# Performance work log

Measured on AMD Instinct MI355X. Metric: run time of the kernel, lower is better.

Reference implementation:

```python
import jax, jax.numpy as jnp
import numpy as np

N, D_IN, D_OUT, H = 8192, 256, 128, 2
SLOPE = 0.2
EPS = 1e-5  # InstanceNorm2d default eps


def setup_inputs() -> dict:
    key = jax.random.key(0)
    ks = jax.random.split(key, 6)
    x = jax.random.normal(ks[0], (N, D_IN), dtype=jnp.float32)
    conn_mask = jnp.where(jax.random.uniform(ks[1], (N, N)) < 0.05, 0.0, -1e9).astype(jnp.float32)
    W = jax.random.normal(ks[2], (H, D_IN, D_OUT), dtype=jnp.float32) * 0.05
    a_src = jax.random.normal(ks[3], (H, D_OUT), dtype=jnp.float32) * 0.1
    a_tgt = jax.random.normal(ks[4], (H, D_OUT), dtype=jnp.float32) * 0.1
    W_res = jax.random.normal(ks[5], (D_OUT, D_IN), dtype=jnp.float32) * 0.05
    return {"x": x, "conn_mask": conn_mask, "W": W, "a_src": a_src, "a_tgt": a_tgt, "W_res": W_res}


def reference(x, conn_mask, W, a_src, a_tgt, W_res):
    # dropout is identity in eval mode
    proj = jnp.einsum('nd,hdf->hnf', x, W)                      # [H,N,F]
    s_src = jnp.einsum('hnf,hf->hn', proj, a_src)[:, :, None]   # [H,N,1]
    s_tgt = jnp.einsum('hnf,hf->hn', proj, a_tgt)[:, None, :]   # [H,1,N]
    scores = jax.nn.leaky_relu(s_src + s_tgt, negative_slope=SLOPE)  # [H,N,N]
    attn = jax.nn.softmax(conn_mask[None] + scores, axis=1)     # softmax over dim=1 as in torch code
    vals = jnp.einsum('hmn,hnf->hmf', attn, proj)               # bmm -> [H,N,F]
    vals = vals.mean(axis=0)                                    # head mean -> [N,F]
    # InstanceNorm2d(1, affine=False) over the whole [N,F] plane, biased variance
    mu = vals.mean()
    var = jnp.mean(jnp.square(vals - mu))
    vals_norm = (vals - mu) / jnp.sqrt(var + EPS)
    out = vals_norm + x @ W_res.T                               # residual projection (no bias)
    out = jax.nn.elu(out)
    return (out, conn_mask)
```

## Files before the change

### kernel.cpp

```cpp
#include <hip/hip_runtime.h>
#include <stdint.h>

#define NN   8192
#define DIN  256
#define FF   128
#define NF   (NN*FF)
#define SLOPE 0.2f
#define EPSI  1e-5f
#define LOG2E 1.4426950408889634f

typedef float vf4 __attribute__((ext_vector_type(4)));
typedef short bf16x8 __attribute__((ext_vector_type(8)));
typedef float f32x4 __attribute__((ext_vector_type(4)));

#define OFF_PROJ   0
#define OFF_RESID  (2*NF)
#define OFF_PACKED (3*NF)
#define OFF_SS     (4*NF)
#define OFF_ST     (OFF_SS + 2*NN)
#define OFF_CSUM   (OFF_ST + 2*NN)
#define OFF_STATS  (OFF_CSUM + 2*NN)
#define OFF_NTAB   (OFF_STATS + 16)
#define OFF_VALS   (OFF_NTAB + 4*NN)
#define OFF_WT     (OFF_VALS + NF)
#define OFF_PT2    (OFF_WT + DIN*FF)
#define OFF_VPART  (OFF_PT2 + NF)

__device__ __forceinline__ float lrelu(float x) { return x >= 0.f ? x : SLOPE * x; }

__device__ __forceinline__ float exp2fast(float x) { return __builtin_amdgcn_exp2f(x); }

__device__ __forceinline__ uint32_t bfpack(float a, float b) {
  uint32_t ua = __float_as_uint(a); ua += 0x7fffu + ((ua >> 16) & 1u);
  uint32_t ub = __float_as_uint(b); ub += 0x7fffu + ((ub >> 16) & 1u);
  return (ua >> 16) | (ub & 0xffff0000u);
}

__global__ __launch_bounds__(256) void k_wt(const float* __restrict__ wres, float* __restrict__ wt) {
  int i = blockIdx.x * 256 + threadIdx.x;
  int d = i >> 7, f = i & 127;
  wt[i] = wres[f * DIN + d];
}

__global__ __launch_bounds__(256) void k_gemm(const float* __restrict__ x, const float* __restrict__ Wh,
                                              const float* __restrict__ wt, float* __restrict__ proj,
                                              float* __restrict__ resid) {
  const int h = blockIdx.y;
  const float* __restrict__ Wsrc = (h < 2) ? (Wh + h * (DIN * FF)) : wt;
  float* __restrict__ outp = (h < 2) ? (proj + h * NF) : resid;
  const int row0 = blockIdx.x * 32;
  __shared__ float xs[32 * 68];
  const int tid = threadIdx.x;
  const int ft = tid & 31, rt = tid >> 5;
  const int f0 = ft * 4, r0 = rt * 4;
  float acc[4][4];
#pragma unroll
  for (int j = 0; j < 4; ++j)
#pragma unroll
    for (int k = 0; k < 4; ++k) acc[j][k] = 0.f;

  for (int kc = 0; kc < 4; ++kc) {
    const int d0 = kc * 64;
#pragma unroll
    for (int k2 = 0; k2 < 2; ++k2) {
      int i = tid * 4 + k2 * 1024;
      int r = i >> 6, dd = i & 63;
      *(float4*)&xs[r * 68 + dd] = *(const float4*)&x[(row0 + r) * DIN + d0 + dd];
    }
    __syncthreads();
#pragma unroll
    for (int g = 0; g < 16; ++g) {
      const int dd = g * 4;
      float xr[4][4];
#pragma unroll
      for (int j = 0; j < 4; ++j) {
        float4 t = *(const float4*)&xs[(r0 + j) * 68 + dd];
        xr[j][0] = t.x; xr[j][1] = t.y; xr[j][2] = t.z; xr[j][3] = t.w;
      }
#pragma unroll
      for (int i = 0; i < 4; ++i) {
        float4 w = *(const float4*)&Wsrc[(d0 + dd + i) * FF + f0];
#pragma unroll
        for (int j = 0; j < 4; ++j) {
          float xx = xr[j][i];
          acc[j][0] += xx * w.x; acc[j][1] += xx * w.y;
          acc[j][2] += xx * w.z; acc[j][3] += xx * w.w;
        }
      }
    }
    __syncthreads();
  }
#pragma unroll
  for (int j = 0; j < 4; ++j) {
    int row = row0 + r0 + j;
    *(float4*)&outp[row * FF + f0] = make_float4(acc[j][0], acc[j][1], acc[j][2], acc[j][3]);
  }
}

__global__ __launch_bounds__(256) void k_sprep(const float* __restrict__ proj, const float* __restrict__ a_src,
                                               const float* __restrict__ a_tgt, float* __restrict__ ss,
                                               float* __restrict__ st, uint32_t* __restrict__ packed) {
  int lane = threadIdx.x & 63, wid = threadIdx.x >> 6;
  int n = blockIdx.x * 4 + wid;
  float2 q0 = *(const float2*)&proj[n * FF + 2 * lane];
  float2 q1 = *(const float2*)&proj[NF + n * FF + 2 * lane];
  float2 as0 = *(const float2*)&a_src[2 * lane];
  float2 at0 = *(const float2*)&a_tgt[2 * lane];
  float2 as1 = *(const float2*)&a_src[FF + 2 * lane];
  float2 at1 = *(const float2*)&a_tgt[FF + 2 * lane];
  float v0 = q0.x * as0.x + q0.y * as0.y;
  float v1 = q0.x * at0.x + q0.y * at0.y;
  float v2 = q1.x * as1.x + q1.y * as1.y;
  float v3 = q1.x * at1.x + q1.y * at1.y;
#pragma unroll
  for (int o = 1; o < 64; o <<= 1) {
    v0 += __shfl_xor(v0, o); v1 += __shfl_xor(v1, o);
    v2 += __shfl_xor(v2, o); v3 += __shfl_xor(v3, o);
  }
  uint2 pk;
  pk.x = bfpack(q0.x, q1.x);
  pk.y = bfpack(q0.y, q1.y);
  *(uint2*)&packed[n * FF + 2 * lane] = pk;
  if (lane == 0) { ss[n] = v0; ss[NN + n] = v2; st[n] = v1; st[NN + n] = v3; }
}

__global__ __launch_bounds__(256) void k_tpose(const uint32_t* __restrict__ packed, uint32_t* __restrict__ pt2) {
  __shared__ uint32_t sb[32][129];
  const int t = threadIdx.x, c = blockIdx.x;
  const int nl = t >> 3, fb = (t & 7) * 16;
#pragma unroll
  for (int i = 0; i < 4; ++i) {
    uint4 v = *(const uint4*)&packed[(c * 32 + nl) * FF + fb + i * 4];
    sb[nl][fb + i * 4] = v.x; sb[nl][fb + i * 4 + 1] = v.y;
    sb[nl][fb + i * 4 + 2] = v.z; sb[nl][fb + i * 4 + 3] = v.w;
  }
  __syncthreads();
  const int h = t >> 7, f = t & 127;
  uint32_t wbuf[16];
#pragma unroll
  for (int p = 0; p < 16; ++p) {
    uint32_t a = sb[2 * p][f], b = sb[2 * p + 1][f];
    wbuf[p] = h ? ((a >> 16) | (b & 0xffff0000u)) : ((a & 0xffffu) | (b << 16));
  }
  uint32_t* dst = pt2 + ((c * 2 + h) * 128 + f) * 16;
#pragma unroll
  for (int i = 0; i < 4; ++i)
    *(uint4*)&dst[i * 4] = make_uint4(wbuf[i * 4], wbuf[i * 4 + 1], wbuf[i * 4 + 2], wbuf[i * 4 + 3]);
}

__global__ __launch_bounds__(256) void k_scan(const float* __restrict__ mask, float* __restrict__ maskout,
                                              const float* __restrict__ ss, const float* __restrict__ st,
                                              float* __restrict__ csum, uint32_t* __restrict__ bitmask) {
  const int tid = threadIdx.x;
  const int lane = tid & 63, wv = tid >> 6;
  const int n = blockIdx.x * 256 + tid;
  const int m0 = blockIdx.y * 128;
  const int wbase = blockIdx.x * 8 + wv * 2;
  const float st0 = st[n] * LOG2E, st1 = st[NN + n] * LOG2E;
  const float ssA = ss[m0 + lane] * LOG2E,      ssB = ss[m0 + 64 + lane] * LOG2E;
  const float ssC = ss[NN + m0 + lane] * LOG2E, ssD = ss[NN + m0 + 64 + lane] * LOG2E;
  float c0 = 0.f, c1 = 0.f;

  for (int i = 0; i < 128; i += 8) {
    float v[8];
#pragma unroll
    for (int r = 0; r < 8; ++r)
      v[r] = __builtin_nontemporal_load(&mask[(size_t)(m0 + i + r) * NN + n]);
#pragma unroll
    for (int r = 0; r < 8; ++r) {
      const int m = m0 + i + r;
      __builtin_nontemporal_store(v[r], &maskout[(size_t)m * NN + n]);
      bool e = v[r] > -0.5e9f;
      unsigned long long bm = __ballot(e);
      if (lane == 0)
        *(uint2*)&bitmask[m * 256 + wbase] = make_uint2((uint32_t)bm, (uint32_t)(bm >> 32));
      const int ri = i + r;
      float s0 = __uint_as_float(__builtin_amdgcn_readlane(
                   __float_as_uint(ri < 64 ? ssA : ssB), ri & 63));
      float s1 = __uint_as_float(__builtin_amdgcn_readlane(
                   __float_as_uint(ri < 64 ? ssC : ssD), ri & 63));
      float w0 = exp2fast(lrelu(s0 + st0));
      float w1 = exp2fast(lrelu(s1 + st1));
      c0 += e ? w0 : 0.f;
      c1 += e ? w1 : 0.f;
    }
  }
  atomicAdd(&csum[n], c0);
  atomicAdd(&csum[NN + n], c1);
}

__global__ __launch_bounds__(256) void k_ntab(const float* __restrict__ st, const float* __restrict__ csum,
                                              float4* __restrict__ ntab) {
  int i = blockIdx.x * 256 + threadIdx.x;
  ntab[i] = make_float4(st[i] * LOG2E, st[NN + i] * LOG2E, 1.f / csum[i], 1.f / csum[NN + i]);
}

__global__ __launch_bounds__(256) void k_vals(const uint32_t* __restrict__ bitmask, const uint32_t* __restrict__ pt2,
                                              const float4* __restrict__ ntab, const float* __restrict__ ss,
                                              float* __restrict__ vpart) {
  __shared__ short B2[2][8][4][16][8];
  __shared__ short A2[2][8][4][16][8];
  const int t = threadIdx.x;
  const int lane = t & 63, wid = t >> 6;
  const int m0 = blockIdx.x * 128;
  const int nc = blockIdx.y;
  const int q = lane >> 4, col = lane & 15;
  const int n2 = t & 15, mg = t >> 4;
  const int fr = t & 127, hB = t >> 7;

  float ssm0[8], ssm1[8];
#pragma unroll
  for (int p = 0; p < 8; ++p) {
    ssm0[p] = ss[m0 + mg + 16 * p] * LOG2E;
    ssm1[p] = ss[NN + m0 + mg + 16 * p] * LOG2E;
  }

  f32x4 acc[2][8];
#pragma unroll
  for (int i = 0; i < 2; ++i)
#pragma unroll
    for (int j = 0; j < 8; ++j) acc[i][j] = (f32x4){0.f, 0.f, 0.f, 0.f};

  uint32_t* B2w = (uint32_t*)&B2[0][0][0][0][0];
  uint32_t* A2w = (uint32_t*)&A2[0][0][0][0][0];

  for (int s = 0; s < 32; ++s) {
    const int n0 = nc * 1024 + s * 32;
    const uint32_t* src = pt2 + (nc * 32 + s) * 4096;
    {
      const uint4* p4 = (const uint4*)&src[t * 16];
#pragma unroll
      for (int k = 0; k < 4; ++k) {
        uint4 v = p4[k];
        *(uint4*)&B2w[(((hB * 8 + (fr >> 4)) * 4 + k) * 16 + (fr & 15)) * 4] = v;
      }
    }
    float4 na = ntab[n0 + 2 * n2];
    float4 nb = ntab[n0 + 2 * n2 + 1];
#pragma unroll
    for (int p = 0; p < 8; ++p) {
      const int ml = mg + 16 * p;
      uint32_t bw = bitmask[(size_t)(m0 + ml) * 256 + (n0 >> 5)];
      float e0a = exp2fast(lrelu(ssm0[p] + na.x)) * na.z;
      float e1a = exp2fast(lrelu(ssm1[p] + na.y)) * na.w;
      float e0b = exp2fast(lrelu(ssm0[p] + nb.x)) * nb.z;
      float e1b = exp2fast(lrelu(ssm1[p] + nb.y)) * nb.w;
      bool b0 = (bw >> (2 * n2)) & 1, b1 = (bw >> (2 * n2 + 1)) & 1;
      e0a = b0 ? e0a : 0.f; e1a = b0 ? e1a : 0.f;
      e0b = b1 ? e0b : 0.f; e1b = b1 ? e1b : 0.f;
      int base = (p * 4 + (n2 >> 2)) * 64 + mg * 4 + (n2 & 3);
      A2w[base] = bfpack(e0a, e0b);
      A2w[base + 2048] = bfpack(e1a, e1b);
    }
    __syncthreads();
    bf16x8 a00 = *(const bf16x8*)&A2[0][wid * 2][q][col][0];
    bf16x8 a01 = *(const bf16x8*)&A2[0][wid * 2 + 1][q][col][0];
    bf16x8 a10 = *(const bf16x8*)&A2[1][wid * 2][q][col][0];
    bf16x8 a11 = *(const bf16x8*)&A2[1][wid * 2 + 1][q][col][0];
#pragma unroll
    for (int ft = 0; ft < 8; ++ft) {
      bf16x8 b0 = *(const bf16x8*)&B2[0][ft][q][col][0];
      acc[0][ft] = __builtin_amdgcn_mfma_f32_16x16x32_bf16(a00, b0, acc[0][ft], 0, 0, 0);
      acc[1][ft] = __builtin_amdgcn_mfma_f32_16x16x32_bf16(a01, b0, acc[1][ft], 0, 0, 0);
      bf16x8 b1 = *(const bf16x8*)&B2[1][ft][q][col][0];
      acc[0][ft] = __builtin_amdgcn_mfma_f32_16x16x32_bf16(a10, b1, acc[0][ft], 0, 0, 0);
      acc[1][ft] = __builtin_amdgcn_mfma_f32_16x16x32_bf16(a11, b1, acc[1][ft], 0, 0, 0);
    }
    __syncthreads();
  }

  float* dst = vpart + (size_t)nc * NF;
#pragma unroll
  for (int mt2 = 0; mt2 < 2; ++mt2)
#pragma unroll
    for (int ft = 0; ft < 8; ++ft)
#pragma unroll
      for (int r = 0; r < 4; ++r) {
        int mrow = m0 + (wid * 2 + mt2) * 16 + q * 4 + r;
        dst[mrow * FF + ft * 16 + col] = 0.5f * acc[mt2][ft][r];
      }
}

__global__ __launch_bounds__(256) void k_stats(const float* __restrict__ vpart, float* __restrict__ vals,
                                               float* __restrict__ stats) {
  int i = (blockIdx.x * 256 + threadIdx.x) * 4;
  float4 a = make_float4(0.f, 0.f, 0.f, 0.f);
#pragma unroll
  for (int p = 0; p < 8; ++p) {
    float4 v = *(const float4*)&vpart[(size_t)p * NF + i];
    a.x += v.x; a.y += v.y; a.z += v.z; a.w += v.w;
  }
  *(float4*)&vals[i] = a;
  float s = a.x + a.y + a.z + a.w;
  float q = a.x * a.x + a.y * a.y + a.z * a.z + a.w * a.w;
#pragma unroll
  for (int o = 1; o < 64; o <<= 1) { s += __shfl_xor(s, o); q += __shfl_xor(q, o); }
  if ((threadIdx.x & 63) == 0) { atomicAdd(stats, s); atomicAdd(stats + 1, q); }
}

__global__ __launch_bounds__(256) void k_final(const float* __restrict__ vals, const float* __restrict__ resid,
                                               const float* __restrict__ stats, float* __restrict__ out) {
  int i = (blockIdx.x * 256 + threadIdx.x) * 4;
  float mu = stats[0] * (1.f / NF);
  float var = stats[1] * (1.f / NF) - mu * mu;
  float rs = rsqrtf(var + EPSI);
  float4 v = *(const float4*)&vals[i];
  float4 r = *(const float4*)&resid[i];
  float t0 = (v.x - mu) * rs + r.x;
  float t1 = (v.y - mu) * rs + r.y;
  float t2 = (v.z - mu) * rs + r.z;
  float t3 = (v.w - mu) * rs + r.w;
  float4 o;
  o.x = t0 > 0.f ? t0 : expm1f(t0);
  o.y = t1 > 0.f ? t1 : expm1f(t1);
  o.z = t2 > 0.f ? t2 : expm1f(t2);
  o.w = t3 > 0.f ? t3 : expm1f(t3);
  *(float4*)&out[i] = o;
}

extern "C" void kernel_launch(void* const* d_in, const int* in_sizes, int n_in,
                              void* d_out, int out_size, void* d_ws, size_t ws_size,
                              hipStream_t stream) {
  const float* x     = (const float*)d_in[0];
  const float* mask  = (const float*)d_in[1];
  const float* W     = (const float*)d_in[2];
  const float* a_src = (const float*)d_in[3];
  const float* a_tgt = (const float*)d_in[4];
  const float* wres  = (const float*)d_in[5];
  float* out = (float*)d_out;
  float* wsf = (float*)d_ws;

  float*    proj    = wsf + OFF_PROJ;
  uint32_t* bitmask = (uint32_t*)(wsf + OFF_PROJ);
  float*    resid   = wsf + OFF_RESID;
  uint32_t* packed  = (uint32_t*)(wsf + OFF_PACKED);
  float*    ss      = wsf + OFF_SS;
  float*    st      = wsf + OFF_ST;
  float*    csum    = wsf + OFF_CSUM;
  float*    stats   = wsf + OFF_STATS;
  float4*   ntab    = (float4*)(wsf + OFF_NTAB);
  float*    vals    = wsf + OFF_VALS;
  float*    wt      = wsf + OFF_WT;
  uint32_t* pt2     = (uint32_t*)(wsf + OFF_PT2);
  float*    vpart   = wsf + OFF_VPART;

  (void)hipMemsetAsync(csum, 0, (2 * NN + 16) * sizeof(float), stream);

  hipLaunchKernelGGL(k_wt,    dim3(DIN * FF / 256), dim3(256), 0, stream, wres, wt);
  hipLaunchKernelGGL(k_gemm,  dim3(NN / 32, 3),     dim3(256), 0, stream, x, W, wt, proj, resid);
  hipLaunchKernelGGL(k_sprep, dim3(NN / 4),         dim3(256), 0, stream, proj, a_src, a_tgt, ss, st, packed);
  hipLaunchKernelGGL(k_tpose, dim3(NN / 32),        dim3(256), 0, stream, packed, pt2);
  hipLaunchKernelGGL(k_scan,  dim3(NN / 256, NN / 128), dim3(256), 0, stream, mask, out + NF, ss, st, csum, bitmask);
  hipLaunchKernelGGL(k_ntab,  dim3(NN / 256),       dim3(256), 0, stream, st, csum, ntab);
  hipLaunchKernelGGL(k_vals,  dim3(NN / 128, 8),    dim3(256), 0, stream, bitmask, pt2, ntab, ss, vpart);
  hipLaunchKernelGGL(k_stats, dim3(NF / 1024),      dim3(256), 0, stream, vpart, vals, stats);
  hipLaunchKernelGGL(k_final, dim3(NF / 1024),      dim3(256), 0, stream, vals, resid, stats, out);
}
```

Measured before the change: 706.2 us.

## Precompute W·a vectors and fuse projection GEMM with mask scan kernel

Attention score vectors are now computed directly from x using precomputed W·a_src and W·a_tgt vectors, so the scores no longer depend on the projection GEMM. The three-output GEMM, bf16 packing and transpose are merged into one block path that writes pt2 directly. That path shares a single launch with the mask scan blocks so the compute-bound GEMM can overlap the bandwidth-bound mask copy. This removes the k_sprep and k_tpose launches and the intermediate proj and packed buffers. The cost is extra shared memory and register pressure in the fused kernel, plus a small reordering of the floating-point sums for the scores.

```diff
diff --git a/kernel.cpp b/kernel.cpp
--- a/kernel.cpp
+++ b/kernel.cpp
@@ -8,14 +8,14 @@
 #define SLOPE 0.2f
 #define EPSI  1e-5f
 #define LOG2E 1.4426950408889634f
-
-typedef float vf4 __attribute__((ext_vector_type(4)));
+#define GEMMB 256
+
 typedef short bf16x8 __attribute__((ext_vector_type(8)));
 typedef float f32x4 __attribute__((ext_vector_type(4)));
 
-#define OFF_PROJ   0
+#define OFF_BM     0
 #define OFF_RESID  (2*NF)
-#define OFF_PACKED (3*NF)
+#define OFF_AVEC   (3*NF)
 #define OFF_SS     (4*NF)
 #define OFF_ST     (OFF_SS + 2*NN)
 #define OFF_CSUM   (OFF_ST + 2*NN)
@@ -36,28 +36,110 @@
   return (ua >> 16) | (ub & 0xffff0000u);
 }
 
-__global__ __launch_bounds__(256) void k_wt(const float* __restrict__ wres, float* __restrict__ wt) {
-  int i = blockIdx.x * 256 + threadIdx.x;
-  int d = i >> 7, f = i & 127;
-  wt[i] = wres[f * DIN + d];
-}
-
-__global__ __launch_bounds__(256) void k_gemm(const float* __restrict__ x, const float* __restrict__ Wh,
-                                              const float* __restrict__ wt, float* __restrict__ proj,
-                                              float* __restrict__ resid) {
-  const int h = blockIdx.y;
-  const float* __restrict__ Wsrc = (h < 2) ? (Wh + h * (DIN * FF)) : wt;
-  float* __restrict__ outp = (h < 2) ? (proj + h * NF) : resid;
-  const int row0 = blockIdx.x * 32;
+__global__ __launch_bounds__(256) void k_prep(const float* __restrict__ wres, float* __restrict__ wtr,
+                                              const float* __restrict__ W, const float* __restrict__ a_src,
+                                              const float* __restrict__ a_tgt, float* __restrict__ avec) {
+  const int b = blockIdx.x;
+  if (b < 128) {
+    int i = b * 256 + threadIdx.x;
+    int d = i >> 7, f = i & 127;
+    wtr[i] = wres[f * DIN + d];
+  } else {
+    int j = b - 128;
+    int h = j & 1, tg = j >> 1;
+    const float* a = (tg ? a_tgt : a_src) + h * FF;
+    const float* Wp = W + ((size_t)h * DIN + threadIdx.x) * FF;
+    float s = 0.f;
+#pragma unroll 8
+    for (int f = 0; f < FF; ++f) s += Wp[f] * a[f];
+    avec[j * DIN + threadIdx.x] = s;
+  }
+}
+
+__global__ __launch_bounds__(256) void k_ss(const float* __restrict__ x, const float* __restrict__ avec,
+                                            float* __restrict__ ss, float* __restrict__ st) {
+  const int lane = threadIdx.x & 63, wid = threadIdx.x >> 6;
+  const int n = blockIdx.x * 4 + wid;
+  float4 xv = *(const float4*)&x[n * DIN + 4 * lane];
+  float4 c0 = *(const float4*)&avec[0 * DIN + 4 * lane];
+  float4 c1 = *(const float4*)&avec[1 * DIN + 4 * lane];
+  float4 c2 = *(const float4*)&avec[2 * DIN + 4 * lane];
+  float4 c3 = *(const float4*)&avec[3 * DIN + 4 * lane];
+  float v0 = xv.x * c0.x + xv.y * c0.y + xv.z * c0.z + xv.w * c0.w;
+  float v1 = xv.x * c1.x + xv.y * c1.y + xv.z * c1.z + xv.w * c1.w;
+  float v2 = xv.x * c2.x + xv.y * c2.y + xv.z * c2.z + xv.w * c2.w;
+  float v3 = xv.x * c3.x + xv.y * c3.y + xv.z * c3.z + xv.w * c3.w;
+#pragma unroll
+  for (int o = 1; o < 64; o <<= 1) {
+    v0 += __shfl_xor(v0, o); v1 += __shfl_xor(v1, o);
+    v2 += __shfl_xor(v2, o); v3 += __shfl_xor(v3, o);
+  }
+  if (lane == 0) { ss[n] = v0; ss[NN + n] = v1; st[n] = v2; st[NN + n] = v3; }
+}
+
+__global__ __launch_bounds__(256) void k_fused(const float* __restrict__ mask, float* __restrict__ maskout,
+                                               const float* __restrict__ ss, const float* __restrict__ st,
+                                               float* __restrict__ csum, uint32_t* __restrict__ bitmask,
+                                               const float* __restrict__ x, const float* __restrict__ Wh,
+                                               const float* __restrict__ wtr, uint32_t* __restrict__ pt2,
+                                               float* __restrict__ resid) {
   __shared__ float xs[32 * 68];
+  __shared__ uint32_t pw[32][129];
+  const int b = blockIdx.x;
   const int tid = threadIdx.x;
+
+  if (b >= GEMMB) {
+    const int bc = b - GEMMB;
+    const int bx = bc & 31, by = bc >> 5;
+    const int lane = tid & 63, wv = tid >> 6;
+    const int n = bx * 256 + tid;
+    const int m0 = by * 128;
+    const int wbase = bx * 8 + wv * 2;
+    const float st0 = st[n] * LOG2E, st1 = st[NN + n] * LOG2E;
+    const float ssA = ss[m0 + lane] * LOG2E,      ssB = ss[m0 + 64 + lane] * LOG2E;
+    const float ssC = ss[NN + m0 + lane] * LOG2E, ssD = ss[NN + m0 + 64 + lane] * LOG2E;
+    float c0 = 0.f, c1 = 0.f;
+
+    for (int i = 0; i < 128; i += 8) {
+      float v[8];
+#pragma unroll
+      for (int r = 0; r < 8; ++r)
+        v[r] = __builtin_nontemporal_load(&mask[(size_t)(m0 + i + r) * NN + n]);
+#pragma unroll
+      for (int r = 0; r < 8; ++r) {
+        const int m = m0 + i + r;
+        __builtin_nontemporal_store(v[r], &maskout[(size_t)m * NN + n]);
+        bool e = v[r] > -0.5e9f;
+        unsigned long long bm = __ballot(e);
+        if (lane == 0)
+          *(uint2*)&bitmask[m * 256 + wbase] = make_uint2((uint32_t)bm, (uint32_t)(bm >> 32));
+        const int ri = i + r;
+        float s0 = __uint_as_float(__builtin_amdgcn_readlane(
+                     __float_as_uint(ri < 64 ? ssA : ssB), ri & 63));
+        float s1 = __uint_as_float(__builtin_amdgcn_readlane(
+                     __float_as_uint(ri < 64 ? ssC : ssD), ri & 63));
+        float w0 = exp2fast(lrelu(s0 + st0));
+        float w1 = exp2fast(lrelu(s1 + st1));
+        c0 += e ? w0 : 0.f;
+        c1 += e ? w1 : 0.f;
+      }
+    }
+    atomicAdd(&csum[n], c0);
+    atomicAdd(&csum[NN + n], c1);
+    return;
+  }
+
+  const int row0 = b * 32;
   const int ft = tid & 31, rt = tid >> 5;
   const int f0 = ft * 4, r0 = rt * 4;
-  float acc[4][4];
+  float a0[4][4], a1[4][4], a2[4][4];
 #pragma unroll
   for (int j = 0; j < 4; ++j)
 #pragma unroll
-    for (int k = 0; k < 4; ++k) acc[j][k] = 0.f;
+    for (int k = 0; k < 4; ++k) { a0[j][k] = 0.f; a1[j][k] = 0.f; a2[j][k] = 0.f; }
+
+  const float* __restrict__ W0 = Wh;
+  const float* __restrict__ W1 = Wh + DIN * FF;
 
   for (int kc = 0; kc < 4; ++kc) {
     const int d0 = kc * 64;
@@ -79,114 +161,52 @@
       }
 #pragma unroll
       for (int i = 0; i < 4; ++i) {
-        float4 w = *(const float4*)&Wsrc[(d0 + dd + i) * FF + f0];
+        const int wrow = (d0 + dd + i) * FF + f0;
+        float4 w = *(const float4*)&W0[wrow];
 #pragma unroll
         for (int j = 0; j < 4; ++j) {
           float xx = xr[j][i];
-          acc[j][0] += xx * w.x; acc[j][1] += xx * w.y;
-          acc[j][2] += xx * w.z; acc[j][3] += xx * w.w;
+          a0[j][0] += xx * w.x; a0[j][1] += xx * w.y; a0[j][2] += xx * w.z; a0[j][3] += xx * w.w;
         }
+        w = *(const float4*)&W1[wrow];
+#pragma unroll
+        for (int j = 0; j < 4; ++j) {
+          float xx = xr[j][i];
+          a1[j][0] += xx * w.x; a1[j][1] += xx * w.y; a1[j][2] += xx * w.z; a1[j][3] += xx * w.w;
+        }
+        w = *(const float4*)&wtr[wrow];
+#pragma unroll
+        for (int j = 0; j < 4; ++j) {
+          float xx = xr[j][i];
+          a2[j][0] += xx * w.x; a2[j][1] += xx * w.y; a2[j][2] += xx * w.z; a2[j][3] += xx * w.w;
+        }
       }
     }
     __syncthreads();
   }
-#pragma unroll
-  for (int j = 0; j < 4; ++j) {
-    int row = row0 + r0 + j;
-    *(float4*)&outp[row * FF + f0] = make_float4(acc[j][0], acc[j][1], acc[j][2], acc[j][3]);
-  }
-}
-
-__global__ __launch_bounds__(256) void k_sprep(const float* __restrict__ proj, const float* __restrict__ a_src,
-                                               const float* __restrict__ a_tgt, float* __restrict__ ss,
-                                               float* __restrict__ st, uint32_t* __restrict__ packed) {
-  int lane = threadIdx.x & 63, wid = threadIdx.x >> 6;
-  int n = blockIdx.x * 4 + wid;
-  float2 q0 = *(const float2*)&proj[n * FF + 2 * lane];
-  float2 q1 = *(const float2*)&proj[NF + n * FF + 2 * lane];
-  float2 as0 = *(const float2*)&a_src[2 * lane];
-  float2 at0 = *(const float2*)&a_tgt[2 * lane];
-  float2 as1 = *(const float2*)&a_src[FF + 2 * lane];
-  float2 at1 = *(const float2*)&a_tgt[FF + 2 * lane];
-  float v0 = q0.x * as0.x + q0.y * as0.y;
-  float v1 = q0.x * at0.x + q0.y * at0.y;
-  float v2 = q1.x * as1.x + q1.y * as1.y;
-  float v3 = q1.x * at1.x + q1.y * at1.y;
-#pragma unroll
-  for (int o = 1; o < 64; o <<= 1) {
-    v0 += __shfl_xor(v0, o); v1 += __shfl_xor(v1, o);
-    v2 += __shfl_xor(v2, o); v3 += __shfl_xor(v3, o);
-  }
-  uint2 pk;
-  pk.x = bfpack(q0.x, q1.x);
-  pk.y = bfpack(q0.y, q1.y);
-  *(uint2*)&packed[n * FF + 2 * lane] = pk;
-  if (lane == 0) { ss[n] = v0; ss[NN + n] = v2; st[n] = v1; st[NN + n] = v3; }
-}
-
-__global__ __launch_bounds__(256) void k_tpose(const uint32_t* __restrict__ packed, uint32_t* __restrict__ pt2) {
-  __shared__ uint32_t sb[32][129];
-  const int t = threadIdx.x, c = blockIdx.x;
-  const int nl = t >> 3, fb = (t & 7) * 16;
-#pragma unroll
-  for (int i = 0; i < 4; ++i) {
-    uint4 v = *(const uint4*)&packed[(c * 32 + nl) * FF + fb + i * 4];
-    sb[nl][fb + i * 4] = v.x; sb[nl][fb + i * 4 + 1] = v.y;
-    sb[nl][fb + i * 4 + 2] = v.z; sb[nl][fb + i * 4 + 3] = v.w;
-  }
+
+#pragma unroll
+  for (int j = 0; j < 4; ++j)
+    *(float4*)&resid[(row0 + r0 + j) * FF + f0] = make_float4(a2[j][0], a2[j][1], a2[j][2], a2[j][3]);
+
+#pragma unroll
+  for (int j = 0; j < 4; ++j)
+#pragma unroll
+    for (int k = 0; k < 4; ++k)
+      pw[r0 + j][f0 + k] = bfpack(a0[j][k], a1[j][k]);
   __syncthreads();
-  const int h = t >> 7, f = t & 127;
+
+  const int h = tid >> 7, f = tid & 127;
   uint32_t wbuf[16];
 #pragma unroll
   for (int p = 0; p < 16; ++p) {
-    uint32_t a = sb[2 * p][f], b = sb[2 * p + 1][f];
-    wbuf[p] = h ? ((a >> 16) | (b & 0xffff0000u)) : ((a & 0xffffu) | (b << 16));
-  }
-  uint32_t* dst = pt2 + ((c * 2 + h) * 128 + f) * 16;
+    uint32_t A = pw[2 * p][f], B = pw[2 * p + 1][f];
+    wbuf[p] = h ? ((A >> 16) | (B & 0xffff0000u)) : ((A & 0xffffu) | (B << 16));
+  }
+  uint32_t* dst = pt2 + ((b * 2 + h) * 128 + f) * 16;
 #pragma unroll
   for (int i = 0; i < 4; ++i)
     *(uint4*)&dst[i * 4] = make_uint4(wbuf[i * 4], wbuf[i * 4 + 1], wbuf[i * 4 + 2], wbuf[i * 4 + 3]);
-}
-
-__global__ __launch_bounds__(256) void k_scan(const float* __restrict__ mask, float* __restrict__ maskout,
-                                              const float* __restrict__ ss, const float* __restrict__ st,
-                                              float* __restrict__ csum, uint32_t* __restrict__ bitmask) {
-  const int tid = threadIdx.x;
-  const int lane = tid & 63, wv = tid >> 6;
-  const int n = blockIdx.x * 256 + tid;
-  const int m0 = blockIdx.y * 128;
-  const int wbase = blockIdx.x * 8 + wv * 2;
-  const float st0 = st[n] * LOG2E, st1 = st[NN + n] * LOG2E;
-  const float ssA = ss[m0 + lane] * LOG2E,      ssB = ss[m0 + 64 + lane] * LOG2E;
-  const float ssC = ss[NN + m0 + lane] * LOG2E, ssD = ss[NN + m0 + 64 + lane] * LOG2E;
-  float c0 = 0.f, c1 = 0.f;
-
-  for (int i = 0; i < 128; i += 8) {
-    float v[8];
-#pragma unroll
-    for (int r = 0; r < 8; ++r)
-      v[r] = __builtin_nontemporal_load(&mask[(size_t)(m0 + i + r) * NN + n]);
-#pragma unroll
-    for (int r = 0; r < 8; ++r) {
-      const int m = m0 + i + r;
-      __builtin_nontemporal_store(v[r], &maskout[(size_t)m * NN + n]);
-      bool e = v[r] > -0.5e9f;
-      unsigned long long bm = __ballot(e);
-      if (lane == 0)
-        *(uint2*)&bitmask[m * 256 + wbase] = make_uint2((uint32_t)bm, (uint32_t)(bm >> 32));
-      const int ri = i + r;
-      float s0 = __uint_as_float(__builtin_amdgcn_readlane(
-                   __float_as_uint(ri < 64 ? ssA : ssB), ri & 63));
-      float s1 = __uint_as_float(__builtin_amdgcn_readlane(
-                   __float_as_uint(ri < 64 ? ssC : ssD), ri & 63));
-      float w0 = exp2fast(lrelu(s0 + st0));
-      float w1 = exp2fast(lrelu(s1 + st1));
-      c0 += e ? w0 : 0.f;
-      c1 += e ? w1 : 0.f;
-    }
-  }
-  atomicAdd(&csum[n], c0);
-  atomicAdd(&csum[NN + n], c1);
 }
 
 __global__ __launch_bounds__(256) void k_ntab(const float* __restrict__ st, const float* __restrict__ csum,
@@ -330,10 +350,9 @@
   float* out = (float*)d_out;
   float* wsf = (float*)d_ws;
 
-  float*    proj    = wsf + OFF_PROJ;
-  uint32_t* bitmask = (uint32_t*)(wsf + OFF_PROJ);
+  uint32_t* bitmask = (uint32_t*)(wsf + OFF_BM);
   float*    resid   = wsf + OFF_RESID;
-  uint32_t* packed  = (uint32_t*)(wsf + OFF_PACKED);
+  float*    avec    = wsf + OFF_AVEC;
   float*    ss      = wsf + OFF_SS;
   float*    st      = wsf + OFF_ST;
   float*    csum    = wsf + OFF_CSUM;
@@ -346,13 +365,12 @@
 
   (void)hipMemsetAsync(csum, 0, (2 * NN + 16) * sizeof(float), stream);
 
-  hipLaunchKernelGGL(k_wt,    dim3(DIN * FF / 256), dim3(256), 0, stream, wres, wt);
-  hipLaunchKernelGGL(k_gemm,  dim3(NN / 32, 3),     dim3(256), 0, stream, x, W, wt, proj, resid);
-  hipLaunchKernelGGL(k_sprep, dim3(NN / 4),         dim3(256), 0, stream, proj, a_src, a_tgt, ss, st, packed);
-  hipLaunchKernelGGL(k_tpose, dim3(NN / 32),        dim3(256), 0, stream, packed, pt2);
-  hipLaunchKernelGGL(k_scan,  dim3(NN / 256, NN / 128), dim3(256), 0, stream, mask, out + NF, ss, st, csum, bitmask);
-  hipLaunchKernelGGL(k_ntab,  dim3(NN / 256),       dim3(256), 0, stream, st, csum, ntab);
-  hipLaunchKernelGGL(k_vals,  dim3(NN / 128, 8),    dim3(256), 0, stream, bitmask, pt2, ntab, ss, vpart);
-  hipLaunchKernelGGL(k_stats, dim3(NF / 1024),      dim3(256), 0, stream, vpart, vals, stats);
-  hipLaunchKernelGGL(k_final, dim3(NF / 1024),      dim3(256), 0, stream, vals, resid, stats, out);
-}
+  hipLaunchKernelGGL(k_prep,  dim3(132),           dim3(256), 0, stream, wres, wt, W, a_src, a_tgt, avec);
+  hipLaunchKernelGGL(k_ss,    dim3(NN / 4),        dim3(256), 0, stream, x, avec, ss, st);
+  hipLaunchKernelGGL(k_fused, dim3(GEMMB + 2048),  dim3(256), 0, stream,
+                     mask, out + NF, ss, st, csum, bitmask, x, W, wt, pt2, resid);
+  hipLaunchKernelGGL(k_ntab,  dim3(NN / 256),      dim3(256), 0, stream, st, csum, ntab);
+  hipLaunchKernelGGL(k_vals,  dim3(NN / 128, 8),   dim3(256), 0, stream, bitmask, pt2, ntab, ss, vpart);
+  hipLaunchKernelGGL(k_stats, dim3(NF / 1024),     dim3(256), 0, stream, vpart, vals, stats);
+  hipLaunchKernelGGL(k_final, dim3(NF / 1024),     dim3(256), 0, stream, vals, resid, stats, out);
+}
```

Result: no change. 719.2 us (+1.8%).
